# Performance work log

Hardware: AMD Instinct MI355X
Metric: run time of the kernel (lower is better)

The kernel has to match this reference:

```python
import jax, jax.numpy as jnp
import numpy as np

B, S, E, H, DH = 4, 2048, 2048, 16, 256  # DH = mlp hidden (d_hid)
HD = E // H  # per-head dim = 128
EPS = 1e-5

def _ln(x, w, b):
    m = jnp.mean(x, axis=-1, keepdims=True)
    v = jnp.mean(jnp.square(x - m), axis=-1, keepdims=True)
    return (x - m) * jax.lax.rsqrt(v + EPS) * w + b

def setup_inputs() -> dict:
    key = jax.random.key(0)
    ks = jax.random.split(key, 10)
    s = 0.02
    return {
        "x": jax.random.normal(ks[0], (B, S, E), jnp.float32),
        "attention_mask": jax.random.randint(ks[1], (B, S), 0, 2, jnp.int32),
        "ln1_w": jnp.ones((E,), jnp.float32),
        "ln1_b": jnp.zeros((E,), jnp.float32),
        "in_proj_w": jax.random.normal(ks[2], (3 * E, E), jnp.float32) * s,
        "in_proj_b": jnp.zeros((3 * E,), jnp.float32),
        "out_proj_w": jax.random.normal(ks[3], (E, E), jnp.float32) * s,
        "out_proj_b": jnp.zeros((E,), jnp.float32),
        "ln2_w": jnp.ones((E,), jnp.float32),
        "ln2_b": jnp.zeros((E,), jnp.float32),
        "mlp_w1": jax.random.normal(ks[4], (DH, E), jnp.float32) * s,
        "mlp_b1": jnp.zeros((DH,), jnp.float32),
        "mlp_w2": jax.random.normal(ks[5], (E, DH), jnp.float32) * s,
        "mlp_b2": jnp.zeros((E,), jnp.float32),
    }

def reference(x, attention_mask, ln1_w, ln1_b, in_proj_w, in_proj_b,
              out_proj_w, out_proj_b, ln2_w, ln2_b, mlp_w1, mlp_b1, mlp_w2, mlp_b2):
    h = _ln(x, ln1_w, ln1_b)
    qkv = h @ in_proj_w.T + in_proj_b  # [B,S,3E]
    q, k, v = jnp.split(qkv, 3, axis=-1)
    q = q.reshape(B, S, H, HD).transpose(0, 2, 1, 3) / jnp.sqrt(jnp.float32(HD))
    k = k.reshape(B, S, H, HD).transpose(0, 2, 1, 3)
    v = v.reshape(B, S, H, HD).transpose(0, 2, 1, 3)
    scores = jnp.einsum("bhqd,bhkd->bhqk", q, k)
    # Faithful to source: FLOAT attn_mask of +1.0 on strictly-upper triangle (additive),
    # NOT -inf; key_padding_mask positions do get -inf.
    causal_add = jnp.triu(jnp.ones((S, S), jnp.float32), k=1)
    scores = scores + causal_add
    pad = (attention_mask == 0)  # True = padded key
    scores = jnp.where(pad[:, None, None, :], jnp.float32(-jnp.inf), scores)
    attn = jax.nn.softmax(scores, axis=-1)
    ctx = jnp.einsum("bhqk,bhkd->bhqd", attn, v)
    ctx = ctx.transpose(0, 2, 1, 3).reshape(B, S, E)
    x = x + ctx @ out_proj_w.T + out_proj_b
    h2 = _ln(x, ln2_w, ln2_b)
    mlp = jax.nn.relu(h2 @ mlp_w1.T + mlp_b1) @ mlp_w2.T + mlp_b2
    return x + mlp
```

## Files before the change

### kernel.cpp

```cpp
#include <hip/hip_runtime.h>

typedef __attribute__((ext_vector_type(8))) short short8;
typedef __attribute__((ext_vector_type(4))) float f32x4;
typedef __attribute__((ext_vector_type(16))) float f32x16;

typedef __attribute__((address_space(1))) const void gas1_t;
typedef __attribute__((address_space(3))) void las3_t;
#define GLL16(g, l) __builtin_amdgcn_global_load_lds((gas1_t*)(g), (las3_t*)(l), 16, 0, 0)

__device__ inline unsigned short f2bf(float f) {
  union { float f; unsigned int u; } v; v.f = f;
  unsigned int r = v.u + 0x7FFFu + ((v.u >> 16) & 1u);
  return (unsigned short)(r >> 16);
}

__device__ inline float exp2_fast(float x) {
  float r; asm("v_exp_f32 %0, %1" : "=v"(r) : "v"(x)); return r;
}

__device__ inline void vmwait(int n) {
  if (n == 6)      asm volatile("s_waitcnt vmcnt(6)" ::: "memory");
  else             asm volatile("s_waitcnt vmcnt(0)" ::: "memory");
}

__global__ __launch_bounds__(256) void ln_kernel(const float* __restrict__ x,
                                                 const float* __restrict__ w,
                                                 const float* __restrict__ bia,
                                                 unsigned short* __restrict__ out) {
  const int row = blockIdx.x;
  const int tid = threadIdx.x;
  const float* xr = x + (size_t)row * 2048;
  float4 a = *(const float4*)(xr + tid * 8);
  float4 b = *(const float4*)(xr + tid * 8 + 4);
  float s  = a.x + a.y + a.z + a.w + b.x + b.y + b.z + b.w;
  float s2 = a.x*a.x + a.y*a.y + a.z*a.z + a.w*a.w + b.x*b.x + b.y*b.y + b.z*b.z + b.w*b.w;
  #pragma unroll
  for (int off = 1; off < 64; off <<= 1) {
    s  += __shfl_xor(s, off);
    s2 += __shfl_xor(s2, off);
  }
  __shared__ float red[8];
  if ((tid & 63) == 0) { red[tid >> 6] = s; red[4 + (tid >> 6)] = s2; }
  __syncthreads();
  s  = red[0] + red[1] + red[2] + red[3];
  s2 = red[4] + red[5] + red[6] + red[7];
  const float mean = s * (1.f / 2048.f);
  const float var  = s2 * (1.f / 2048.f) - mean * mean;
  const float rstd = rsqrtf(var + 1e-5f);
  float4 wa = *(const float4*)(w + tid * 8), wb = *(const float4*)(w + tid * 8 + 4);
  float4 ba = *(const float4*)(bia + tid * 8), bb = *(const float4*)(bia + tid * 8 + 4);
  short8 o;
  o[0] = (short)f2bf((a.x - mean) * rstd * wa.x + ba.x);
  o[1] = (short)f2bf((a.y - mean) * rstd * wa.y + ba.y);
  o[2] = (short)f2bf((a.z - mean) * rstd * wa.z + ba.z);
  o[3] = (short)f2bf((a.w - mean) * rstd * wa.w + ba.w);
  o[4] = (short)f2bf((b.x - mean) * rstd * wb.x + bb.x);
  o[5] = (short)f2bf((b.y - mean) * rstd * wb.y + bb.y);
  o[6] = (short)f2bf((b.z - mean) * rstd * wb.z + bb.z);
  o[7] = (short)f2bf((b.w - mean) * rstd * wb.w + bb.w);
  *(short8*)(out + (size_t)row * 2048 + tid * 8) = o;
}

__global__ __launch_bounds__(256) void conv_kernel(const float* __restrict__ in,
                                                   unsigned short* __restrict__ out, int n) {
  size_t idx = ((size_t)blockIdx.x * 256 + threadIdx.x) * 8;
  if (idx >= (size_t)n) return;
  float4 a = *(const float4*)(in + idx);
  float4 b = *(const float4*)(in + idx + 4);
  short8 o;
  o[0] = (short)f2bf(a.x); o[1] = (short)f2bf(a.y);
  o[2] = (short)f2bf(a.z); o[3] = (short)f2bf(a.w);
  o[4] = (short)f2bf(b.x); o[5] = (short)f2bf(b.y);
  o[6] = (short)f2bf(b.z); o[7] = (short)f2bf(b.w);
  *(short8*)(out + idx) = o;
}

template <int MODE>
__global__ __launch_bounds__(256) void gemm_bt(const unsigned short* __restrict__ A,
                                               const unsigned short* __restrict__ Bw,
                                               const float* __restrict__ bias,
                                               const float* __restrict__ res,
                                               void* __restrict__ outp,
                                               void* __restrict__ outp2,
                                               int M, int N, int K) {
  __shared__ unsigned short As[128 * 64];
  __shared__ unsigned short Bs[128 * 64];
  const int tid = threadIdx.x;
  const int l = tid & 63, wv = tid >> 6;
  const int l15 = l & 15, l4 = l >> 4;
  const int wr = wv >> 1, wc = wv & 1;
  const int nx = gridDim.x;
  const int nwg = nx * gridDim.y;
  const int bidlin = blockIdx.y * nx + blockIdx.x;
  const int cpx = nwg >> 3;
  const int swz = (bidlin & 7) * cpx + (bidlin >> 3);
  const int m0 = (swz / nx) * 128, n0 = (swz % nx) * 128;

  f32x4 acc[4][4] = {};
  for (int k0 = 0; k0 < K; k0 += 64) {
    __syncthreads();
    #pragma unroll
    for (int i = 0; i < 4; ++i) {
      int e = i * 2048 + tid * 8;
      int r = e >> 6;
      int c = (e ^ ((r & 7) << 3)) & 63;
      GLL16(A + (size_t)(m0 + r) * K + k0 + c, As + e);
      GLL16(Bw + (size_t)(n0 + r) * K + k0 + c, Bs + e);
    }
    __syncthreads();
    #pragma unroll
    for (int kk = 0; kk < 64; kk += 32) {
      short8 af[4], bfr[4];
      #pragma unroll
      for (int m = 0; m < 4; ++m) {
        int r = wr * 64 + m * 16 + l15;
        int byt = (r * 128 + (kk + l4 * 8) * 2) ^ ((r & 7) << 4);
        af[m] = *(const short8*)((const char*)As + byt);
      }
      #pragma unroll
      for (int n = 0; n < 4; ++n) {
        int r = wc * 64 + n * 16 + l15;
        int byt = (r * 128 + (kk + l4 * 8) * 2) ^ ((r & 7) << 4);
        bfr[n] = *(const short8*)((const char*)Bs + byt);
      }
      #pragma unroll
      for (int m = 0; m < 4; ++m)
        #pragma unroll
        for (int n = 0; n < 4; ++n)
          acc[m][n] = __builtin_amdgcn_mfma_f32_16x16x32_bf16(af[m], bfr[n], acc[m][n], 0, 0, 0);
    }
  }
  #pragma unroll
  for (int m = 0; m < 4; ++m) {
    #pragma unroll
    for (int n = 0; n < 4; ++n) {
      #pragma unroll
      for (int r = 0; r < 4; ++r) {
        int row = m0 + wr * 64 + m * 16 + l4 * 4 + r;
        int col = n0 + wc * 64 + n * 16 + l15;
        float v = acc[m][n][r] + bias[col];
        if (MODE == 1) {
          ((unsigned short*)outp)[(size_t)row * N + col] = f2bf(v > 0.f ? v : 0.f);
        } else {
          ((float*)outp)[(size_t)row * N + col] = res[(size_t)row * N + col] + v;
        }
      }
    }
  }
}

template <int MODE>
__global__ __launch_bounds__(512, 2) void gemm8(const unsigned short* __restrict__ A,
                                                const unsigned short* __restrict__ Bw,
                                                const float* __restrict__ bias,
                                                const float* __restrict__ res,
                                                void* __restrict__ outp,
                                                void* __restrict__ outp2,
                                                int M, int N, int K) {
  __shared__ char LA[2][2][16384];
  __shared__ char LB[2][2][16384];
  const int tid = threadIdx.x;
  const int l = tid & 63, wv = tid >> 6;
  const int l15 = l & 15, l4 = l >> 4;
  const int wr = wv >> 2, wc = wv & 3;
  const int wch = wc >> 1, wcl = wc & 1;
  const int nx = gridDim.x;
  const int nwg = nx * gridDim.y;
  const int bidlin = blockIdx.y * nx + blockIdx.x;
  const int cpx = nwg >> 3;
  const int swz = (bidlin & 7) * cpx + (bidlin >> 3);
  const int m0 = (swz / nx) * 256, n0 = (swz % nx) * 256;

  const int srow = tid >> 3;
  const int scol = ((tid & 7) ^ (srow & 7)) * 8;

#define STG_A(x, h) { const unsigned short* bp = A + (size_t)(m0 + (h) * 128) * K + (x) * 64; \
    GLL16(bp + (size_t)srow * K + scol, &LA[(x) & 1][h][tid * 16]); \
    GLL16(bp + (size_t)(srow + 64) * K + scol, &LA[(x) & 1][h][8192 + tid * 16]); }
#define STG_B(x, h) { const unsigned short* bp = Bw + (size_t)(n0 + (h) * 128) * K + (x) * 64; \
    GLL16(bp + (size_t)srow * K + scol, &LB[(x) & 1][h][tid * 16]); \
    GLL16(bp + (size_t)(srow + 64) * K + scol, &LB[(x) & 1][h][8192 + tid * 16]); }

#define FOFF(r, kh) ((r) * 128 + (((((kh) * 4 + l4)) ^ ((r) & 7)) << 4))

  f32x4 acc[8][4] = {};
  const int NT = K >> 6;

  STG_A(0, 0); STG_A(0, 1); STG_B(0, 0); STG_B(0, 1);
  STG_B(1, 0); STG_B(1, 1); STG_A(1, 0);
  vmwait(6);
  __builtin_amdgcn_s_barrier();

#define MFMAQ(mh, nh) \
    __builtin_amdgcn_s_setprio(1); \
    _Pragma("unroll") for (int kh = 0; kh < 2; ++kh) \
      _Pragma("unroll") for (int f = 0; f < 4; ++f) \
        _Pragma("unroll") for (int n = 0; n < 2; ++n) \
          acc[(mh) * 4 + f][(nh) * 2 + n] = __builtin_amdgcn_mfma_f32_16x16x32_bf16( \
              af[kh][f], bfr[kh][(nh) * 2 + n], acc[(mh) * 4 + f][(nh) * 2 + n], 0, 0, 0); \
    __builtin_amdgcn_s_setprio(0);

  for (int t = 0; t < NT; ++t) {
    const char* Ab = LA[t & 1][wr];
    const char* Bb = LB[t & 1][wch];
    short8 af[2][4], bfr[2][4];
    #pragma unroll
    for (int kh = 0; kh < 2; ++kh)
      #pragma unroll
      for (int f = 0; f < 4; ++f) {
        af[kh][f] = *(const short8*)(Ab + FOFF(f * 16 + l15, kh));
        bfr[kh][f] = *(const short8*)(Bb + FOFF(wcl * 64 + f * 16 + l15, kh));
      }
    if (t + 1 < NT) STG_A(t + 1, 1);
    __builtin_amdgcn_s_barrier();
    asm volatile("s_waitcnt lgkmcnt(0)" ::: "memory");
    __builtin_amdgcn_sched_barrier(0);
    MFMAQ(0, 0);
    MFMAQ(0, 1);
    __builtin_amdgcn_s_barrier();
    #pragma unroll
    for (int kh = 0; kh < 2; ++kh)
      #pragma unroll
      for (int f = 0; f < 4; ++f)
        af[kh][f] = *(const short8*)(Ab + FOFF(64 + f * 16 + l15, kh));
    if (t + 2 < NT) { STG_B(t + 2, 0); STG_B(t + 2, 1); STG_A(t + 2, 0); }
    __builtin_amdgcn_s_barrier();
    asm volatile("s_waitcnt lgkmcnt(0)" ::: "memory");
    __builtin_amdgcn_sched_barrier(0);
    MFMAQ(1, 0);
    MFMAQ(1, 1);
    vmwait(t >= NT - 2 ? 0 : 6);
    __builtin_amdgcn_s_barrier();
  }
#undef MFMAQ
#undef FOFF
#undef STG_A
#undef STG_B

  #pragma unroll
  for (int mf = 0; mf < 8; ++mf) {
    #pragma unroll
    for (int nf = 0; nf < 4; ++nf) {
      #pragma unroll
      for (int r = 0; r < 4; ++r) {
        int row = m0 + wr * 128 + mf * 16 + l4 * 4 + r;
        int col = n0 + wc * 64 + nf * 16 + l15;
        float v = acc[mf][nf][r] + bias[col];
        if (MODE == 0) {
          unsigned short val = f2bf(v);
          if (col < 4096) ((unsigned short*)outp)[(size_t)row * 4096 + col] = val;
          else            ((unsigned short*)outp2)[(size_t)row * 2048 + col - 4096] = val;
        } else {
          ((float*)outp)[(size_t)row * N + col] = res[(size_t)row * N + col] + v;
        }
      }
    }
  }
}

__global__ __launch_bounds__(256) void vtrans_kernel(const unsigned short* __restrict__ v,
                                                     unsigned short* __restrict__ vT) {
  __shared__ unsigned short T[128 * 128];
  const int t0 = blockIdx.x * 128;
  const int b = blockIdx.y >> 4, h = blockIdx.y & 15;
  const int tid = threadIdx.x;
  const int tl = tid >> 4, l16 = tid & 15, c8 = l16 * 8;
  #pragma unroll
  for (int i = 0; i < 8; ++i) {
    int t = tl + i * 16;
    short8 val = *(const short8*)(v + (size_t)(b * 2048 + t0 + t) * 2048 + h * 128 + c8);
    *(short8*)((char*)T + ((t * 256 + c8 * 2) ^ ((t & 7) << 4))) = val;
  }
  __syncthreads();
  #pragma unroll
  for (int i = 0; i < 8; ++i) {
    int d = tl + i * 16;
    unsigned short* orow = vT + ((size_t)(b * 16 + h) * 128 + d) * 2048 + t0;
    #pragma unroll
    for (int j = 0; j < 8; ++j) {
      int t = l16 + 16 * j;
      orow[t] = *(const unsigned short*)((const char*)T + ((t * 256 + d * 2) ^ ((t & 7) << 4)));
    }
  }
}

__global__ __launch_bounds__(256) void attn_kernel(const unsigned short* __restrict__ qk,
                                                   const unsigned short* __restrict__ vT,
                                                   const int* __restrict__ amask,
                                                   unsigned short* __restrict__ ctx) {
  __shared__ unsigned short Ks[2][4096];
  __shared__ unsigned short Vs[2][4096];

  const int lin = blockIdx.y * 16 + blockIdx.x;
  const int swzb = (lin & 7) * 128 + (lin >> 3);
  const int qt = swzb & 15, bh = swzb >> 4;
  const int b = bh >> 4, h = bh & 15;
  const int tid = threadIdx.x;
  const int wv = tid >> 6, l = tid & 63;
  const int l31 = l & 31, hi = l >> 5;
  const int q0w = qt * 128 + wv * 32;
  const float SC2 = 0.08838834764831845f * 1.4426950408889634f;
  const float L2E = 1.4426950408889634f;
  const float MF  = 10.0f;

  int kinv[2], vinv[2];
  #pragma unroll
  for (int c = 0; c < 2; ++c) {
    int e = c * 2048 + tid * 8;
    int key = e >> 7, d0 = e & 127;
    kinv[c] = key * 4096 + 2048 + h * 128 + (d0 ^ ((key & 7) << 3));
    int d = e >> 5, kchunk = ((e >> 3) & 3) ^ ((d & 6) >> 1);
    vinv[c] = d * 2048 + kchunk * 8;
  }
  const unsigned short* kb0 = qk + (size_t)(b * 2048) * 4096;
  const unsigned short* vb0 = vT + (size_t)(b * 16 + h) * (128 * 2048);
  const int* mrow = amask + b * 2048;

  short8 qf[8];
  {
    const unsigned short* qp = qk + (size_t)(b * 2048 + q0w + l31) * 4096 + h * 128 + hi * 8;
    #pragma unroll
    for (int c = 0; c < 8; ++c) qf[c] = *(const short8*)(qp + c * 16);
  }

  short8 vones;
  #pragma unroll
  for (int j = 0; j < 8; ++j) vones[j] = (short)0x3F80;

  f32x16 o[4] = {};
  f32x16 ol = {};

  #pragma unroll
  for (int c = 0; c < 2; ++c) {
    GLL16(kb0 + kinv[c], &Ks[0][c * 2048 + tid * 8]);
    GLL16(vb0 + vinv[c], &Vs[0][c * 2048 + tid * 8]);
  }
  __syncthreads();

  for (int kt = 0; kt < 2048; kt += 32) {
    const int cur = (kt >> 5) & 1;
    if (kt + 32 < 2048) {
      #pragma unroll
      for (int c = 0; c < 2; ++c) {
        GLL16(kb0 + (size_t)(kt + 32) * 4096 + kinv[c], &Ks[cur ^ 1][c * 2048 + tid * 8]);
        GLL16(vb0 + (kt + 32) + vinv[c], &Vs[cur ^ 1][c * 2048 + tid * 8]);
      }
    }
    const unsigned bm = (unsigned)__ballot((l < 32) && (mrow[kt + l31] == 0));
    const unsigned bmh = bm >> (4 * hi);

    f32x16 sacc = {};
    __builtin_amdgcn_s_setprio(1);
    #pragma unroll
    for (int c = 0; c < 8; ++c) {
      short8 kf = *(const short8*)((const char*)Ks[cur] +
                   ((l31 * 256 + c * 32 + hi * 16) ^ ((l31 & 7) << 4)));
      sacc = __builtin_amdgcn_mfma_f32_32x32x16_bf16(kf, qf[c], sacc, 0, 0, 0);
    }
    __builtin_amdgcn_s_setprio(0);

    const int Dq = q0w + l31 - kt - 4 * hi;
    float p[16];
    if (kt > q0w + 31) {
      #pragma unroll
      for (int i = 0; i < 16; ++i) p[i] = sacc[i] * SC2 + (L2E - MF);
    } else if (kt + 31 <= q0w) {
      #pragma unroll
      for (int i = 0; i < 16; ++i) p[i] = sacc[i] * SC2 - MF;
    } else {
      #pragma unroll
      for (int i = 0; i < 16; ++i) {
        const int ci = (i & 3) + 8 * (i >> 2);
        p[i] = sacc[i] * SC2 + ((ci > Dq) ? (L2E - MF) : -MF);
      }
    }
    #pragma unroll
    for (int i = 0; i < 16; ++i) {
      const int ci = (i & 3) + 8 * (i >> 2);
      if ((bmh >> ci) & 1) p[i] = -1e30f;
    }
    #pragma unroll
    for (int i = 0; i < 16; ++i) p[i] = exp2_fast(p[i]);

#define CVTPK(dst, a, bsrc) asm("v_cvt_pk_bf16_f32 %0, %1, %2" : "=v"(dst) : "v"(a), "v"(bsrc))
#define PLSWAP(fst, snd) asm("v_permlane32_swap_b32 %0, %1" : "+v"(fst), "+v"(snd))
    unsigned x, x2, y, y2, u, u2, v, v2;
    CVTPK(x,  p[0],  p[1]);  CVTPK(x2, p[2],  p[3]);
    CVTPK(y,  p[4],  p[5]);  CVTPK(y2, p[6],  p[7]);
    CVTPK(u,  p[8],  p[9]);  CVTPK(u2, p[10], p[11]);
    CVTPK(v,  p[12], p[13]); CVTPK(v2, p[14], p[15]);
    PLSWAP(x, y);  PLSWAP(x2, y2);
    PLSWAP(u, v);  PLSWAP(u2, v2);
    union { unsigned w[4]; short8 s8; } P0, P1;
    P0.w[0] = x; P0.w[1] = x2; P0.w[2] = y; P0.w[3] = y2;
    P1.w[0] = u; P1.w[1] = u2; P1.w[2] = v; P1.w[3] = v2;
    short8 pa0 = P0.s8, pa1 = P1.s8;
#undef CVTPK
#undef PLSWAP

    __builtin_amdgcn_s_setprio(1);
    #pragma unroll
    for (int g = 0; g < 4; ++g) {
      int d = g * 32 + l31;
      int swzd = (d & 6) << 3;
      short8 vf0 = *(const short8*)((const char*)Vs[cur] + ((d * 64 + hi * 16) ^ swzd));
      o[g] = __builtin_amdgcn_mfma_f32_32x32x16_bf16(pa0, vf0, o[g], 0, 0, 0);
      short8 vf1 = *(const short8*)((const char*)Vs[cur] + ((d * 64 + 32 + hi * 16) ^ swzd));
      o[g] = __builtin_amdgcn_mfma_f32_32x32x16_bf16(pa1, vf1, o[g], 0, 0, 0);
    }
    ol = __builtin_amdgcn_mfma_f32_32x32x16_bf16(pa0, vones, ol, 0, 0, 0);
    ol = __builtin_amdgcn_mfma_f32_32x32x16_bf16(pa1, vones, ol, 0, 0, 0);
    __builtin_amdgcn_s_setprio(0);

    __syncthreads();
  }

  float inv[16];
  #pragma unroll
  for (int i = 0; i < 16; ++i) inv[i] = 1.0f / ol[i];
  #pragma unroll
  for (int g = 0; g < 4; ++g) {
    #pragma unroll
    for (int i = 0; i < 16; ++i) {
      int q = q0w + (i & 3) + 8 * (i >> 2) + 4 * hi;
      ctx[(size_t)(b * 2048 + q) * 2048 + h * 128 + g * 32 + l31] = f2bf(o[g][i] * inv[i]);
    }
  }
}

extern "C" void kernel_launch(void* const* d_in, const int* in_sizes, int n_in,
                              void* d_out, int out_size, void* d_ws, size_t ws_size,
                              hipStream_t stream) {
  (void)in_sizes; (void)n_in; (void)out_size; (void)ws_size;
  const float* x    = (const float*)d_in[0];
  const int*   am   = (const int*)d_in[1];
  const float* ln1w = (const float*)d_in[2];
  const float* ln1b = (const float*)d_in[3];
  const float* win  = (const float*)d_in[4];
  const float* bin  = (const float*)d_in[5];
  const float* wout = (const float*)d_in[6];
  const float* bout = (const float*)d_in[7];
  const float* ln2w = (const float*)d_in[8];
  const float* ln2b = (const float*)d_in[9];
  const float* w1   = (const float*)d_in[10];
  const float* b1   = (const float*)d_in[11];
  const float* w2   = (const float*)d_in[12];
  const float* b2   = (const float*)d_in[13];
  float* out = (float*)d_out;

  char* ws = (char*)d_ws;
  unsigned short* hbuf = (unsigned short*)ws;
  unsigned short* vTb  = (unsigned short*)ws;
  unsigned short* qkb  = (unsigned short*)(ws + (size_t)32 * 1048576);
  unsigned short* h2b  = (unsigned short*)(ws + (size_t)32 * 1048576);
  unsigned short* midb = (unsigned short*)(ws + (size_t)64 * 1048576);
  unsigned short* vbuf = (unsigned short*)(ws + (size_t)96 * 1048576);
  unsigned short* ctxb = (unsigned short*)(ws + (size_t)96 * 1048576);
  unsigned short* wbuf = (unsigned short*)(ws + (size_t)128 * 1048576);

  ln_kernel<<<dim3(8192), dim3(256), 0, stream>>>(x, ln1w, ln1b, hbuf);
  conv_kernel<<<dim3(6144), dim3(256), 0, stream>>>(win, wbuf, 12582912);
  gemm8<0><<<dim3(24, 32), dim3(512), 0, stream>>>(hbuf, wbuf, bin, (const float*)nullptr,
                                                   (void*)qkb, (void*)vbuf, 8192, 6144, 2048);
  vtrans_kernel<<<dim3(16, 64), dim3(256), 0, stream>>>(vbuf, vTb);
  attn_kernel<<<dim3(16, 64), dim3(256), 0, stream>>>(qkb, vTb, am, ctxb);
  conv_kernel<<<dim3(2048), dim3(256), 0, stream>>>(wout, wbuf, 4194304);
  gemm8<2><<<dim3(8, 32), dim3(512), 0, stream>>>(ctxb, wbuf, bout, x,
                                                  (void*)out, nullptr, 8192, 2048, 2048);
  ln_kernel<<<dim3(8192), dim3(256), 0, stream>>>(out, ln2w, ln2b, h2b);
  conv_kernel<<<dim3(256), dim3(256), 0, stream>>>(w1, wbuf, 524288);
  gemm_bt<1><<<dim3(2, 64), dim3(256), 0, stream>>>(h2b, wbuf, b1, (const float*)nullptr,
                                                    (void*)midb, nullptr, 8192, 256, 2048);
  conv_kernel<<<dim3(256), dim3(256), 0, stream>>>(w2, wbuf, 524288);
  gemm_bt<2><<<dim3(16, 64), dim3(256), 0, stream>>>(midb, wbuf, b2, out,
                                                     (void*)out, nullptr, 8192, 2048, 256);
}
```

Measured before the change: 608.3 us.

## Split LDS fragment loads by k-half to overlap with MFMAs; use gemm8 for MLP down-projection

The gemm8 main loop now loads LDS fragments in two k-halves. It waits only on the first half (partial lgkmcnt) before starting MFMAs on it, so the second half's LDS reads overlap with compute instead of draining fully first. The MFMA grouping is reorganised by k-half rather than by n-half. The MLP second projection (K=256) also moves from gemm_bt to the larger 256x256-tile gemm8 kernel. That launches fewer, bigger blocks with only 4 k-iterations each, which may hurt occupancy or pipeline fill.

```diff
diff --git a/kernel.cpp b/kernel.cpp
--- a/kernel.cpp
+++ b/kernel.cpp
@@ -191,13 +191,12 @@
   vmwait(6);
   __builtin_amdgcn_s_barrier();
 
-#define MFMAQ(mh, nh) \
+#define MFMAK(mh, kh) \
     __builtin_amdgcn_s_setprio(1); \
-    _Pragma("unroll") for (int kh = 0; kh < 2; ++kh) \
-      _Pragma("unroll") for (int f = 0; f < 4; ++f) \
-        _Pragma("unroll") for (int n = 0; n < 2; ++n) \
-          acc[(mh) * 4 + f][(nh) * 2 + n] = __builtin_amdgcn_mfma_f32_16x16x32_bf16( \
-              af[kh][f], bfr[kh][(nh) * 2 + n], acc[(mh) * 4 + f][(nh) * 2 + n], 0, 0, 0); \
+    _Pragma("unroll") for (int f = 0; f < 4; ++f) \
+      _Pragma("unroll") for (int n = 0; n < 4; ++n) \
+        acc[(mh) * 4 + f][n] = __builtin_amdgcn_mfma_f32_16x16x32_bf16( \
+            af[kh][f], bfr[kh][n], acc[(mh) * 4 + f][n], 0, 0, 0); \
     __builtin_amdgcn_s_setprio(0);
 
   for (int t = 0; t < NT; ++t) {
@@ -205,34 +204,44 @@
     const char* Bb = LB[t & 1][wch];
     short8 af[2][4], bfr[2][4];
     #pragma unroll
-    for (int kh = 0; kh < 2; ++kh)
-      #pragma unroll
-      for (int f = 0; f < 4; ++f) {
-        af[kh][f] = *(const short8*)(Ab + FOFF(f * 16 + l15, kh));
-        bfr[kh][f] = *(const short8*)(Bb + FOFF(wcl * 64 + f * 16 + l15, kh));
-      }
+    for (int f = 0; f < 4; ++f) {
+      bfr[0][f] = *(const short8*)(Bb + FOFF(wcl * 64 + f * 16 + l15, 0));
+      af[0][f]  = *(const short8*)(Ab + FOFF(f * 16 + l15, 0));
+    }
+    __builtin_amdgcn_sched_barrier(0);
+    #pragma unroll
+    for (int f = 0; f < 4; ++f) {
+      bfr[1][f] = *(const short8*)(Bb + FOFF(wcl * 64 + f * 16 + l15, 1));
+      af[1][f]  = *(const short8*)(Ab + FOFF(f * 16 + l15, 1));
+    }
     if (t + 1 < NT) STG_A(t + 1, 1);
     __builtin_amdgcn_s_barrier();
+    asm volatile("s_waitcnt lgkmcnt(8)" ::: "memory");
+    __builtin_amdgcn_sched_barrier(0);
+    MFMAK(0, 0);
     asm volatile("s_waitcnt lgkmcnt(0)" ::: "memory");
     __builtin_amdgcn_sched_barrier(0);
-    MFMAQ(0, 0);
-    MFMAQ(0, 1);
+    MFMAK(0, 1);
     __builtin_amdgcn_s_barrier();
     #pragma unroll
-    for (int kh = 0; kh < 2; ++kh)
-      #pragma unroll
-      for (int f = 0; f < 4; ++f)
-        af[kh][f] = *(const short8*)(Ab + FOFF(64 + f * 16 + l15, kh));
+    for (int f = 0; f < 4; ++f)
+      af[0][f] = *(const short8*)(Ab + FOFF(64 + f * 16 + l15, 0));
+    __builtin_amdgcn_sched_barrier(0);
+    #pragma unroll
+    for (int f = 0; f < 4; ++f)
+      af[1][f] = *(const short8*)(Ab + FOFF(64 + f * 16 + l15, 1));
     if (t + 2 < NT) { STG_B(t + 2, 0); STG_B(t + 2, 1); STG_A(t + 2, 0); }
     __builtin_amdgcn_s_barrier();
+    asm volatile("s_waitcnt lgkmcnt(4)" ::: "memory");
+    __builtin_amdgcn_sched_barrier(0);
+    MFMAK(1, 0);
     asm volatile("s_waitcnt lgkmcnt(0)" ::: "memory");
     __builtin_amdgcn_sched_barrier(0);
-    MFMAQ(1, 0);
-    MFMAQ(1, 1);
+    MFMAK(1, 1);
     vmwait(t >= NT - 2 ? 0 : 6);
     __builtin_amdgcn_s_barrier();
   }
-#undef MFMAQ
+#undef MFMAK
 #undef FOFF
 #undef STG_A
 #undef STG_B
@@ -472,6 +481,6 @@
   gemm_bt<1><<<dim3(2, 64), dim3(256), 0, stream>>>(h2b, wbuf, b1, (const float*)nullptr,
                                                     (void*)midb, nullptr, 8192, 256, 2048);
   conv_kernel<<<dim3(256), dim3(256), 0, stream>>>(w2, wbuf, 524288);
-  gemm_bt<2><<<dim3(16, 64), dim3(256), 0, stream>>>(midb, wbuf, b2, out,
-                                                     (void*)out, nullptr, 8192, 2048, 256);
-}
+  gemm8<2><<<dim3(8, 32), dim3(512), 0, stream>>>(midb, wbuf, b2, out,
+                                                  (void*)out, nullptr, 8192, 2048, 256);
+}
```

Measured after the change: 607.9 us. About the same (-0.1%).
